# Performance work log

Measured on AMD Instinct MI355X. Metric: run time of the kernel, lower is better.

The kernel has to match this reference:

```python
import jax, jax.numpy as jnp
import numpy as np

EMBED_DIM = 1024
MEMORY_SIZE = 64
TOPK = 3
LN_EPS = 1e-5


def setup_inputs() -> dict:
    key = jax.random.key(0)
    ks = jax.random.split(key, 8)
    D, M = EMBED_DIM, MEMORY_SIZE
    scale = 1.0 / np.sqrt(D)
    x = jax.random.normal(ks[0], (8, 2048, D), dtype=jnp.float32)
    memory = jax.random.normal(ks[1], (M, D), dtype=jnp.float32) * scale
    Wq = jax.random.normal(ks[2], (D, D), dtype=jnp.float32) * scale
    bq = jnp.zeros((D,), dtype=jnp.float32)
    Wf = jax.random.normal(ks[3], (D, 2 * D), dtype=jnp.float32) * (1.0 / np.sqrt(2 * D))
    bf = jnp.zeros((D,), dtype=jnp.float32)
    gamma = jnp.ones((D,), dtype=jnp.float32)
    beta = jnp.zeros((D,), dtype=jnp.float32)
    return {"x": x, "memory": memory, "Wq": Wq, "bq": bq,
            "Wf": Wf, "bf": bf, "gamma": gamma, "beta": beta}


def reference(x, memory, Wq, bq, Wf, bf, gamma, beta):
    B, S, D = x.shape
    # query projection: [B,S,D]
    query = jnp.einsum('bsd,ed->bse', x, Wq) + bq
    # similarity to memory bank: [B,S,M]
    sim = jnp.einsum('bsd,md->bsm', query, memory)
    # top-k over memory slots
    topk_sim, topk_idx = jax.lax.top_k(sim, TOPK)            # [B,S,K]
    weights = jax.nn.softmax(topk_sim, axis=-1)               # [B,S,K]
    retrieved = memory[topk_idx]                              # [B,S,K,D]
    memory_output = jnp.einsum('bskd,bsk->bsd', retrieved, weights)
    # fusion MLP: Linear(2D->D) -> LayerNorm -> ReLU
    cat = jnp.concatenate([x, memory_output], axis=-1)        # [B,S,2D]
    h = jnp.einsum('bsc,dc->bsd', cat, Wf) + bf
    mean = jnp.mean(h, axis=-1, keepdims=True)
    var = jnp.mean(jnp.square(h - mean), axis=-1, keepdims=True)
    h = (h - mean) * jax.lax.rsqrt(var + LN_EPS) * gamma + beta
    return jax.nn.relu(h)
```

## Files before the change

### kernel.cpp

```cpp
#include <hip/hip_runtime.h>

#define DCH 1024
#define MSLOT 64
#define NTOK 16384

typedef __bf16 bf16x8 __attribute__((ext_vector_type(8)));
typedef float f32x4 __attribute__((ext_vector_type(4)));
typedef unsigned short u16x8 __attribute__((ext_vector_type(8)));
typedef unsigned short u16x4 __attribute__((ext_vector_type(4)));

__device__ __forceinline__ unsigned short f2bf(float f) {
  unsigned u = __float_as_uint(f);
  u += 0x7fffu + ((u >> 16) & 1u);
  return (unsigned short)(u >> 16);
}
__device__ __forceinline__ float bf2f(unsigned short s) {
  return __uint_as_float(((unsigned)s) << 16);
}

__device__ __forceinline__ void gld16(const void* g, void* l) {
  __builtin_amdgcn_global_load_lds((const __attribute__((address_space(1))) void*)g,
                                   (__attribute__((address_space(3))) void*)l, 16, 0, 0);
}

__global__ __launch_bounds__(256) void prep_a_kernel(
    const float* __restrict__ Wf, float* __restrict__ Wf2T,
    unsigned short* __restrict__ Wf1b,
    const float* __restrict__ bq, const float* __restrict__ memv,
    float* __restrict__ sc) {
  __shared__ float tile[64][65];
  __shared__ float red[256];
  const int b = blockIdx.x, tid = threadIdx.x;

  if (b >= 257) {
    const int j = b - 257;
#pragma unroll
    for (int i = 0; i < 16; ++i) {
      int f4 = j * 4096 + i * 256 + tid;
      int row = f4 >> 8, c4 = (f4 & 255) * 4;
      float4 v = *(const float4*)(Wf + (size_t)row * 2048 + c4);
      u16x4 o = {f2bf(v.x), f2bf(v.y), f2bf(v.z), f2bf(v.w)};
      *(u16x4*)(Wf1b + row * 1024 + c4) = o;
    }
  } else if (b >= 1) {
    const int t = b - 1;
    const int c0 = (t & 15) * 64, d0 = (t >> 4) * 64;
    const int lane = tid & 63, wv = tid >> 6;
#pragma unroll
    for (int i = 0; i < 16; ++i) {
      int r = wv + i * 4;
      tile[r][lane] = Wf[(size_t)(d0 + r) * 2048 + 1024 + c0 + lane];
    }
    __syncthreads();
#pragma unroll
    for (int i = 0; i < 16; ++i) {
      int r = wv + i * 4;
      Wf2T[(size_t)(c0 + r) * 1024 + d0 + lane] = tile[lane][r];
    }
  } else {
    int m = tid >> 2, q = tid & 3;
    float s = 0.f;
    for (int e = q * 256; e < q * 256 + 256; ++e) s += bq[e] * memv[m * 1024 + e];
    red[tid] = s;
    __syncthreads();
    if (tid < 64) sc[tid] = red[tid * 4] + red[tid * 4 + 1] + red[tid * 4 + 2] + red[tid * 4 + 3];
  }
}

__global__ __launch_bounds__(256) void prep_b_kernel(
    const float* __restrict__ memv, const float* __restrict__ Wq,
    const float* __restrict__ Wf2T,
    float* __restrict__ partWm, float* __restrict__ partP) {
  int b = blockIdx.x;
  const int tid = threadIdx.x;
  const int which = b >> 7;
  b &= 127;
  const int kc = b & 7, dt = (b >> 3) & 3, mg = b >> 5;
  const float* B = which ? Wf2T : Wq;
  float* outp = which ? partP : partWm;
  const int d = dt * 256 + tid;
  const int e0 = kc * 128;
  const int m0 = mg * 16;

  float acc[16];
#pragma unroll
  for (int m = 0; m < 16; ++m) acc[m] = 0.f;

  const float* bp = B + (size_t)e0 * 1024 + d;
  const float* mp = memv + m0 * 1024 + e0;
#pragma unroll 4
  for (int e = 0; e < 128; ++e) {
    float wv = bp[(size_t)e * 1024];
#pragma unroll
    for (int m = 0; m < 16; ++m) acc[m] += mp[m * 1024 + e] * wv;
  }
  float* op = outp + ((size_t)kc * 64 + m0) * 1024 + d;
#pragma unroll
  for (int m = 0; m < 16; ++m) op[m * 1024] = acc[m];
}

__global__ __launch_bounds__(256) void prep_c_kernel(
    const float* __restrict__ partWm, const float* __restrict__ partP,
    unsigned short* __restrict__ Wmb, float* __restrict__ P) {
  int idx = blockIdx.x * 256 + threadIdx.x;
  if (idx < 65536) {
    float s = 0.f;
#pragma unroll
    for (int k = 0; k < 8; ++k) s += partWm[k * 65536 + idx];
    Wmb[idx] = f2bf(s);
  } else {
    idx -= 65536;
    float s = 0.f;
#pragma unroll
    for (int k = 0; k < 8; ++k) s += partP[k * 65536 + idx];
    P[idx] = s;
  }
}

__global__ __launch_bounds__(256) void sim_topk_kernel(
    const float* __restrict__ x,
    const unsigned short* __restrict__ Wmb,
    const float* __restrict__ sc, float4* __restrict__ meta) {
  __shared__ __attribute__((aligned(16))) unsigned short As[16 * 64];
  __shared__ __attribute__((aligned(16))) unsigned short Bs[64 * 64];
  __shared__ float sim_s[16 * 65];
  const int tid = threadIdx.x;
  const int wave = tid >> 6, lane = tid & 63;
  const int tok0 = blockIdx.x * 16;
  const int quad = lane >> 4, cl = lane & 15;
  const int sw = ((lane & 7) ^ (lane >> 3)) * 8;
  const int cx0 = ((quad) ^ (cl & 7)) * 8;
  const int cx1 = ((quad + 4) ^ (cl & 7)) * 8;

  const int arow = tid >> 3, acc_ = tid & 7;
  const int alc = acc_ ^ (arow & 7);

  f32x4 acc = {0.f, 0.f, 0.f, 0.f};

  for (int kt = 0; kt < 16; ++kt) {
    __syncthreads();
#pragma unroll
    for (int i = 0; i < 2; ++i) {
      int ch = (wave * 2 + i) * 64 + lane;
      int row = ch >> 3;
      gld16(Wmb + row * 1024 + kt * 64 + sw, Bs + ch * 8);
    }
    if (tid < 128) {
      const size_t goff = (size_t)(tok0 + arow) * 1024 + kt * 64 + alc * 8;
      float4 v0 = *(const float4*)(x + goff);
      float4 v1 = *(const float4*)(x + goff + 4);
      u16x8 o = {f2bf(v0.x), f2bf(v0.y), f2bf(v0.z), f2bf(v0.w),
                 f2bf(v1.x), f2bf(v1.y), f2bf(v1.z), f2bf(v1.w)};
      *(u16x8*)(As + tid * 8) = o;
    }
    __syncthreads();
#pragma unroll
    for (int ks = 0; ks < 2; ++ks) {
      const int cx = ks ? cx1 : cx0;
      bf16x8 a = *(const bf16x8*)(As + cl * 64 + cx);
      bf16x8 bb = *(const bf16x8*)(Bs + (wave * 16 + cl) * 64 + cx);
      acc = __builtin_amdgcn_mfma_f32_16x16x32_bf16(a, bb, acc, 0, 0, 0);
    }
  }
#pragma unroll
  for (int r = 0; r < 4; ++r) {
    int lt = quad * 4 + r;
    int mc = wave * 16 + cl;
    sim_s[lt * 65 + mc] = acc[r] + sc[mc];
  }
  __syncthreads();
  if (tid < 16) {
    const float* sp = sim_s + tid * 65;
    float s0 = -1e30f, s1 = -1e30f, s2 = -1e30f;
    int i0 = 0, i1 = 0, i2 = 0;
    for (int m = 0; m < 64; ++m) {
      float v = sp[m];
      if (v > s0) { s2 = s1; i2 = i1; s1 = s0; i1 = i0; s0 = v; i0 = m; }
      else if (v > s1) { s2 = s1; i2 = i1; s1 = v; i1 = m; }
      else if (v > s2) { s2 = v; i2 = m; }
    }
    float e1 = __expf(s1 - s0), e2 = __expf(s2 - s0);
    float inv = 1.f / (1.f + e1 + e2);
    meta[tok0 + tid] = make_float4(inv, e1 * inv, e2 * inv,
                                   __int_as_float(i0 | (i1 << 8) | (i2 << 16)));
  }
}

__global__ __launch_bounds__(256, 2) void gemm_h_kernel(
    const float* __restrict__ x, const unsigned short* __restrict__ Wf1b,
    unsigned short* __restrict__ hb) {
  __shared__ __attribute__((aligned(16))) unsigned short As[256 * 64];
  __shared__ __attribute__((aligned(16))) unsigned short Bs[128 * 64];
  const int tid = threadIdx.x;
  const int wave = tid >> 6, lane = tid & 63;
  const int b = blockIdx.x;
  const int tok0 = (b & 63) * 256, d0 = (b >> 6) * 128;
  const int quad = lane >> 4, cl = lane & 15;
  const int wm = wave * 64;
  const int sw = ((lane & 7) ^ (lane >> 3)) * 8;
  const int cx0 = ((quad) ^ (cl & 7)) * 8;
  const int cx1 = ((quad + 4) ^ (cl & 7)) * 8;

  const int acc_ = lane & 7, ar3 = lane >> 3;
  const int alc = acc_ ^ ar3;

  f32x4 acc[4][8];
#pragma unroll
  for (int i = 0; i < 4; ++i)
#pragma unroll
    for (int j = 0; j < 8; ++j) acc[i][j] = {0.f, 0.f, 0.f, 0.f};

  for (int kt = 0; kt < 16; ++kt) {
    __syncthreads();
#pragma unroll
    for (int i = 0; i < 8; ++i) {
      int row = (wave * 8 + i) * 8 + ar3;
      const size_t goff = (size_t)(tok0 + row) * 1024 + kt * 64 + alc * 8;
      float4 v0 = *(const float4*)(x + goff);
      float4 v1 = *(const float4*)(x + goff + 4);
      u16x8 o = {f2bf(v0.x), f2bf(v0.y), f2bf(v0.z), f2bf(v0.w),
                 f2bf(v1.x), f2bf(v1.y), f2bf(v1.z), f2bf(v1.w)};
      *(u16x8*)(As + ((wave * 8 + i) * 64 + lane) * 8) = o;
    }
#pragma unroll
    for (int i = 0; i < 4; ++i) {
      int ch = (wave * 4 + i) * 64 + lane;
      int row = ch >> 3;
      gld16(Wf1b + (size_t)(d0 + row) * 1024 + kt * 64 + sw, Bs + ch * 8);
    }
    __syncthreads();
#pragma unroll
    for (int ks = 0; ks < 2; ++ks) {
      const int cx = ks ? cx1 : cx0;
      bf16x8 a[4], bb[8];
#pragma unroll
      for (int t = 0; t < 4; ++t)
        a[t] = *(const bf16x8*)(As + (wm + cl + t * 16) * 64 + cx);
#pragma unroll
      for (int t = 0; t < 8; ++t)
        bb[t] = *(const bf16x8*)(Bs + (cl + t * 16) * 64 + cx);
#pragma unroll
      for (int mt = 0; mt < 4; ++mt)
#pragma unroll
        for (int nt = 0; nt < 8; ++nt)
          acc[mt][nt] = __builtin_amdgcn_mfma_f32_16x16x32_bf16(a[mt], bb[nt], acc[mt][nt], 0, 0, 0);
    }
  }

#pragma unroll
  for (int mt = 0; mt < 4; ++mt) {
#pragma unroll
    for (int r = 0; r < 4; ++r) {
      int row = tok0 + wm + mt * 16 + quad * 4 + r;
#pragma unroll
      for (int nt = 0; nt < 8; ++nt) {
        int d = d0 + nt * 16 + cl;
        hb[(size_t)row * 1024 + d] = f2bf(acc[mt][nt][r]);
      }
    }
  }
}

__global__ __launch_bounds__(256) void ln_relu_kernel(
    const unsigned short* __restrict__ hb, const float* __restrict__ P,
    const float4* __restrict__ meta, const float* __restrict__ bfv,
    const float* __restrict__ gamma, const float* __restrict__ beta,
    float* __restrict__ out) {
  const int tid = threadIdx.x;
  const int wave = tid >> 6, lane = tid & 63;
  const int t = blockIdx.x * 4 + wave;

  float4 mv = meta[t];
  int pk = __float_as_int(mv.w);
  const float* P0 = P + (pk & 255) * 1024;
  const float* P1 = P + ((pk >> 8) & 255) * 1024;
  const float* P2 = P + ((pk >> 16) & 255) * 1024;

  const unsigned short* hp = hb + (size_t)t * 1024;

  u16x4 hv[4];
  float4 b4[4], p0[4], p1[4], p2[4];
#pragma unroll
  for (int j = 0; j < 4; ++j) {
    const int off = (j * 64 + lane) * 4;
    hv[j] = *(const u16x4*)(hp + off);
    b4[j] = *(const float4*)(bfv + off);
    p0[j] = *(const float4*)(P0 + off);
    p1[j] = *(const float4*)(P1 + off);
    p2[j] = *(const float4*)(P2 + off);
  }

  float f[16];
#pragma unroll
  for (int j = 0; j < 4; ++j) {
    f[j * 4 + 0] = bf2f(hv[j][0]) + b4[j].x + mv.x * p0[j].x + mv.y * p1[j].x + mv.z * p2[j].x;
    f[j * 4 + 1] = bf2f(hv[j][1]) + b4[j].y + mv.x * p0[j].y + mv.y * p1[j].y + mv.z * p2[j].y;
    f[j * 4 + 2] = bf2f(hv[j][2]) + b4[j].z + mv.x * p0[j].z + mv.y * p1[j].z + mv.z * p2[j].z;
    f[j * 4 + 3] = bf2f(hv[j][3]) + b4[j].w + mv.x * p0[j].w + mv.y * p1[j].w + mv.z * p2[j].w;
  }
  float s = 0.f, q = 0.f;
#pragma unroll
  for (int j = 0; j < 16; ++j) { s += f[j]; q += f[j] * f[j]; }
#pragma unroll
  for (int off = 32; off; off >>= 1) {
    s += __shfl_xor(s, off);
    q += __shfl_xor(q, off);
  }
  float mean = s * (1.f / 1024.f);
  float var = q * (1.f / 1024.f) - mean * mean;
  float rs = rsqrtf(var + 1e-5f);
  float* op = out + (size_t)t * 1024;
#pragma unroll
  for (int j = 0; j < 4; ++j) {
    const int off = (j * 64 + lane) * 4;
    float4 g4 = *(const float4*)(gamma + off);
    float4 e4 = *(const float4*)(beta + off);
    float4 v;
    v.x = fmaxf((f[j * 4 + 0] - mean) * rs * g4.x + e4.x, 0.f);
    v.y = fmaxf((f[j * 4 + 1] - mean) * rs * g4.y + e4.y, 0.f);
    v.z = fmaxf((f[j * 4 + 2] - mean) * rs * g4.z + e4.z, 0.f);
    v.w = fmaxf((f[j * 4 + 3] - mean) * rs * g4.w + e4.w, 0.f);
    *(float4*)(op + off) = v;
  }
}

extern "C" void kernel_launch(void* const* d_in, const int* in_sizes, int n_in,
                              void* d_out, int out_size, void* d_ws, size_t ws_size,
                              hipStream_t stream) {
  const float* x     = (const float*)d_in[0];
  const float* memv  = (const float*)d_in[1];
  const float* Wq    = (const float*)d_in[2];
  const float* bq    = (const float*)d_in[3];
  const float* Wf    = (const float*)d_in[4];
  const float* bfv   = (const float*)d_in[5];
  const float* gamma = (const float*)d_in[6];
  const float* beta  = (const float*)d_in[7];
  float* out = (float*)d_out;
  char* ws = (char*)d_ws;

  unsigned short* Wf1b   = (unsigned short*)(ws);
  unsigned short* Wmb    = (unsigned short*)(ws + 2097152);
  float*          P      = (float*)(ws + 2228224);
  float*          sc     = (float*)(ws + 2490368);
  float4*         meta   = (float4*)(ws + 2490624);
  float*          Wf2T   = (float*)(ws + 2752768);
  float*          partWm = (float*)(ws + 6947072);
  float*          partP  = (float*)(ws + 9044224);
  unsigned short* hb     = (unsigned short*)(ws + 11141376);

  hipLaunchKernelGGL(prep_a_kernel, dim3(321), dim3(256), 0, stream,
                     Wf, Wf2T, Wf1b, bq, memv, sc);
  hipLaunchKernelGGL(prep_b_kernel, dim3(256), dim3(256), 0, stream,
                     memv, Wq, Wf2T, partWm, partP);
  hipLaunchKernelGGL(prep_c_kernel, dim3(512), dim3(256), 0, stream,
                     partWm, partP, Wmb, P);
  hipLaunchKernelGGL(sim_topk_kernel, dim3(1024), dim3(256), 0, stream,
                     x, Wmb, sc, meta);
  hipLaunchKernelGGL(gemm_h_kernel, dim3(512), dim3(256), 0, stream,
                     x, Wf1b, hb);
  hipLaunchKernelGGL(ln_relu_kernel, dim3(4096), dim3(256), 0, stream,
                     hb, P, meta, bfv, gamma, beta, out);
}
```

Before: 245.6 us.

## Fuse memory-similarity GEMM and partial top-3 into main GEMM kernel

```diff
diff --git a/kernel.cpp b/kernel.cpp
--- a/kernel.cpp
+++ b/kernel.cpp
@@ -117,89 +117,23 @@
   }
 }
 
-__global__ __launch_bounds__(256) void sim_topk_kernel(
-    const float* __restrict__ x,
-    const unsigned short* __restrict__ Wmb,
-    const float* __restrict__ sc, float4* __restrict__ meta) {
-  __shared__ __attribute__((aligned(16))) unsigned short As[16 * 64];
-  __shared__ __attribute__((aligned(16))) unsigned short Bs[64 * 64];
-  __shared__ float sim_s[16 * 65];
-  const int tid = threadIdx.x;
-  const int wave = tid >> 6, lane = tid & 63;
-  const int tok0 = blockIdx.x * 16;
-  const int quad = lane >> 4, cl = lane & 15;
-  const int sw = ((lane & 7) ^ (lane >> 3)) * 8;
-  const int cx0 = ((quad) ^ (cl & 7)) * 8;
-  const int cx1 = ((quad + 4) ^ (cl & 7)) * 8;
-
-  const int arow = tid >> 3, acc_ = tid & 7;
-  const int alc = acc_ ^ (arow & 7);
-
-  f32x4 acc = {0.f, 0.f, 0.f, 0.f};
-
-  for (int kt = 0; kt < 16; ++kt) {
-    __syncthreads();
-#pragma unroll
-    for (int i = 0; i < 2; ++i) {
-      int ch = (wave * 2 + i) * 64 + lane;
-      int row = ch >> 3;
-      gld16(Wmb + row * 1024 + kt * 64 + sw, Bs + ch * 8);
-    }
-    if (tid < 128) {
-      const size_t goff = (size_t)(tok0 + arow) * 1024 + kt * 64 + alc * 8;
-      float4 v0 = *(const float4*)(x + goff);
-      float4 v1 = *(const float4*)(x + goff + 4);
-      u16x8 o = {f2bf(v0.x), f2bf(v0.y), f2bf(v0.z), f2bf(v0.w),
-                 f2bf(v1.x), f2bf(v1.y), f2bf(v1.z), f2bf(v1.w)};
-      *(u16x8*)(As + tid * 8) = o;
-    }
-    __syncthreads();
-#pragma unroll
-    for (int ks = 0; ks < 2; ++ks) {
-      const int cx = ks ? cx1 : cx0;
-      bf16x8 a = *(const bf16x8*)(As + cl * 64 + cx);
-      bf16x8 bb = *(const bf16x8*)(Bs + (wave * 16 + cl) * 64 + cx);
-      acc = __builtin_amdgcn_mfma_f32_16x16x32_bf16(a, bb, acc, 0, 0, 0);
-    }
-  }
-#pragma unroll
-  for (int r = 0; r < 4; ++r) {
-    int lt = quad * 4 + r;
-    int mc = wave * 16 + cl;
-    sim_s[lt * 65 + mc] = acc[r] + sc[mc];
-  }
-  __syncthreads();
-  if (tid < 16) {
-    const float* sp = sim_s + tid * 65;
-    float s0 = -1e30f, s1 = -1e30f, s2 = -1e30f;
-    int i0 = 0, i1 = 0, i2 = 0;
-    for (int m = 0; m < 64; ++m) {
-      float v = sp[m];
-      if (v > s0) { s2 = s1; i2 = i1; s1 = s0; i1 = i0; s0 = v; i0 = m; }
-      else if (v > s1) { s2 = s1; i2 = i1; s1 = v; i1 = m; }
-      else if (v > s2) { s2 = v; i2 = m; }
-    }
-    float e1 = __expf(s1 - s0), e2 = __expf(s2 - s0);
-    float inv = 1.f / (1.f + e1 + e2);
-    meta[tok0 + tid] = make_float4(inv, e1 * inv, e2 * inv,
-                                   __int_as_float(i0 | (i1 << 8) | (i2 << 16)));
-  }
-}
-
 __global__ __launch_bounds__(256, 2) void gemm_h_kernel(
     const float* __restrict__ x, const unsigned short* __restrict__ Wf1b,
-    unsigned short* __restrict__ hb) {
+    const unsigned short* __restrict__ Wmb, const float* __restrict__ sc,
+    unsigned short* __restrict__ hb, float4* __restrict__ psimtop) {
   __shared__ __attribute__((aligned(16))) unsigned short As[256 * 64];
   __shared__ __attribute__((aligned(16))) unsigned short Bs[128 * 64];
+  __shared__ __attribute__((aligned(16))) unsigned short Bs2[16 * 64];
   const int tid = threadIdx.x;
   const int wave = tid >> 6, lane = tid & 63;
   const int b = blockIdx.x;
-  const int tok0 = (b & 63) * 256, d0 = (b >> 6) * 128;
+  const int tok0 = (b & 63) * 256, dt = b >> 6, d0 = dt * 128;
   const int quad = lane >> 4, cl = lane & 15;
   const int wm = wave * 64;
   const int sw = ((lane & 7) ^ (lane >> 3)) * 8;
   const int cx0 = ((quad) ^ (cl & 7)) * 8;
   const int cx1 = ((quad + 4) ^ (cl & 7)) * 8;
+  const bool do_sim = (dt < 4);
 
   const int acc_ = lane & 7, ar3 = lane >> 3;
   const int alc = acc_ ^ ar3;
@@ -209,6 +143,9 @@
   for (int i = 0; i < 4; ++i)
 #pragma unroll
     for (int j = 0; j < 8; ++j) acc[i][j] = {0.f, 0.f, 0.f, 0.f};
+  f32x4 sacc[4];
+#pragma unroll
+  for (int i = 0; i < 4; ++i) sacc[i] = {0.f, 0.f, 0.f, 0.f};
 
   for (int kt = 0; kt < 16; ++kt) {
     __syncthreads();
@@ -228,6 +165,11 @@
       int row = ch >> 3;
       gld16(Wf1b + (size_t)(d0 + row) * 1024 + kt * 64 + sw, Bs + ch * 8);
     }
+    if (do_sim && wave < 2) {
+      int ch = wave * 64 + lane;
+      int row = ch >> 3;
+      gld16(Wmb + (size_t)(dt * 16 + row) * 1024 + kt * 64 + sw, Bs2 + ch * 8);
+    }
     __syncthreads();
 #pragma unroll
     for (int ks = 0; ks < 2; ++ks) {
@@ -244,6 +186,12 @@
 #pragma unroll
         for (int nt = 0; nt < 8; ++nt)
           acc[mt][nt] = __builtin_amdgcn_mfma_f32_16x16x32_bf16(a[mt], bb[nt], acc[mt][nt], 0, 0, 0);
+      if (do_sim) {
+        bf16x8 b2 = *(const bf16x8*)(Bs2 + cl * 64 + cx);
+#pragma unroll
+        for (int mt = 0; mt < 4; ++mt)
+          sacc[mt] = __builtin_amdgcn_mfma_f32_16x16x32_bf16(a[mt], b2, sacc[mt], 0, 0, 0);
+      }
     }
   }
 
@@ -259,23 +207,69 @@
       }
     }
   }
+
+  if (do_sim) {
+    const float scv = sc[dt * 16 + cl];
+#pragma unroll
+    for (int mt = 0; mt < 4; ++mt) {
+#pragma unroll
+      for (int r = 0; r < 4; ++r) {
+        float v0 = sacc[mt][r] + scv;
+        int j0 = dt * 16 + cl;
+        float v1 = -1e30f, v2 = -1e30f;
+        int j1 = 0, j2 = 0;
+#pragma unroll
+        for (int off = 1; off < 16; off <<= 1) {
+          float w0 = __shfl_xor(v0, off), w1 = __shfl_xor(v1, off), w2 = __shfl_xor(v2, off);
+          int k0 = __shfl_xor(j0, off), k1 = __shfl_xor(j1, off), k2 = __shfl_xor(j2, off);
+          if (w0 > v0) { v2 = v1; j2 = j1; v1 = v0; j1 = j0; v0 = w0; j0 = k0; }
+          else if (w0 > v1) { v2 = v1; j2 = j1; v1 = w0; j1 = k0; }
+          else if (w0 > v2) { v2 = w0; j2 = k0; }
+          if (w1 > v1) { v2 = v1; j2 = j1; v1 = w1; j1 = k1; }
+          else if (w1 > v2) { v2 = w1; j2 = k1; }
+          if (w2 > v2) { v2 = w2; j2 = k2; }
+        }
+        if (cl == 0) {
+          int tok = tok0 + wm + mt * 16 + quad * 4 + r;
+          psimtop[(size_t)tok * 4 + dt] =
+              make_float4(v0, v1, v2, __int_as_float(j0 | (j1 << 8) | (j2 << 16)));
+        }
+      }
+    }
+  }
 }
 
 __global__ __launch_bounds__(256) void ln_relu_kernel(
     const unsigned short* __restrict__ hb, const float* __restrict__ P,
-    const float4* __restrict__ meta, const float* __restrict__ bfv,
+    const float4* __restrict__ psimtop, const float* __restrict__ bfv,
     const float* __restrict__ gamma, const float* __restrict__ beta,
     float* __restrict__ out) {
   const int tid = threadIdx.x;
   const int wave = tid >> 6, lane = tid & 63;
   const int t = blockIdx.x * 4 + wave;
 
-  float4 mv = meta[t];
-  int pk = __float_as_int(mv.w);
-  const float* P0 = P + (pk & 255) * 1024;
-  const float* P1 = P + ((pk >> 8) & 255) * 1024;
-  const float* P2 = P + ((pk >> 16) & 255) * 1024;
-
+  float v0 = -1e30f, v1 = -1e30f, v2 = -1e30f;
+  int i0 = 0, i1 = 0, i2 = 0;
+#pragma unroll
+  for (int g = 0; g < 4; ++g) {
+    float4 gv = psimtop[(size_t)t * 4 + g];
+    int pkk = __float_as_int(gv.w);
+    float w0 = gv.x, w1 = gv.y, w2 = gv.z;
+    int k0 = pkk & 255, k1 = (pkk >> 8) & 255, k2 = (pkk >> 16) & 255;
+    if (w0 > v0) { v2 = v1; i2 = i1; v1 = v0; i1 = i0; v0 = w0; i0 = k0; }
+    else if (w0 > v1) { v2 = v1; i2 = i1; v1 = w0; i1 = k0; }
+    else if (w0 > v2) { v2 = w0; i2 = k0; }
+    if (w1 > v1) { v2 = v1; i2 = i1; v1 = w1; i1 = k1; }
+    else if (w1 > v2) { v2 = w1; i2 = k1; }
+    if (w2 > v2) { v2 = w2; i2 = k2; }
+  }
+  float e1 = __expf(v1 - v0), e2 = __expf(v2 - v0);
+  float inv = 1.f / (1.f + e1 + e2);
+  const float wgt0 = inv, wgt1 = e1 * inv, wgt2 = e2 * inv;
+
+  const float* P0 = P + i0 * 1024;
+  const float* P1 = P + i1 * 1024;
+  const float* P2 = P + i2 * 1024;
   const unsigned short* hp = hb + (size_t)t * 1024;
 
   u16x4 hv[4];
@@ -293,10 +287,10 @@
   float f[16];
 #pragma unroll
   for (int j = 0; j < 4; ++j) {
-    f[j * 4 + 0] = bf2f(hv[j][0]) + b4[j].x + mv.x * p0[j].x + mv.y * p1[j].x + mv.z * p2[j].x;
-    f[j * 4 + 1] = bf2f(hv[j][1]) + b4[j].y + mv.x * p0[j].y + mv.y * p1[j].y + mv.z * p2[j].y;
-    f[j * 4 + 2] = bf2f(hv[j][2]) + b4[j].z + mv.x * p0[j].z + mv.y * p1[j].z + mv.z * p2[j].z;
-    f[j * 4 + 3] = bf2f(hv[j][3]) + b4[j].w + mv.x * p0[j].w + mv.y * p1[j].w + mv.z * p2[j].w;
+    f[j * 4 + 0] = bf2f(hv[j][0]) + b4[j].x + wgt0 * p0[j].x + wgt1 * p1[j].x + wgt2 * p2[j].x;
+    f[j * 4 + 1] = bf2f(hv[j][1]) + b4[j].y + wgt0 * p0[j].y + wgt1 * p1[j].y + wgt2 * p2[j].y;
+    f[j * 4 + 2] = bf2f(hv[j][2]) + b4[j].z + wgt0 * p0[j].z + wgt1 * p1[j].z + wgt2 * p2[j].z;
+    f[j * 4 + 3] = bf2f(hv[j][3]) + b4[j].w + wgt0 * p0[j].w + wgt1 * p1[j].w + wgt2 * p2[j].w;
   }
   float s = 0.f, q = 0.f;
 #pragma unroll
@@ -342,11 +336,11 @@
   unsigned short* Wmb    = (unsigned short*)(ws + 2097152);
   float*          P      = (float*)(ws + 2228224);
   float*          sc     = (float*)(ws + 2490368);
-  float4*         meta   = (float4*)(ws + 2490624);
   float*          Wf2T   = (float*)(ws + 2752768);
   float*          partWm = (float*)(ws + 6947072);
   float*          partP  = (float*)(ws + 9044224);
   unsigned short* hb     = (unsigned short*)(ws + 11141376);
+  float4*         psimtop= (float4*)(ws + 44695808);
 
   hipLaunchKernelGGL(prep_a_kernel, dim3(321), dim3(256), 0, stream,
                      Wf, Wf2T, Wf1b, bq, memv, sc);
@@ -354,10 +348,8 @@
                      memv, Wq, Wf2T, partWm, partP);
   hipLaunchKernelGGL(prep_c_kernel, dim3(512), dim3(256), 0, stream,
                      partWm, partP, Wmb, P);
-  hipLaunchKernelGGL(sim_topk_kernel, dim3(1024), dim3(256), 0, stream,
-                     x, Wmb, sc, meta);
   hipLaunchKernelGGL(gemm_h_kernel, dim3(512), dim3(256), 0, stream,
-                     x, Wf1b, hb);
+                     x, Wf1b, Wmb, sc, hb, psimtop);
   hipLaunchKernelGGL(ln_relu_kernel, dim3(4096), dim3(256), 0, stream,
-                     hb, P, meta, bfv, gamma, beta, out);
-}
+                     hb, P, psimtop, bfv, gamma, beta, out);
+}
```

Measured after the change: 288.1 us. 17.3% more time.
